# Performance work log

Measured on AMD Instinct MI355X. Metric: run time of the kernel, lower is better.

The kernel has to match this reference:

```python
import jax, jax.numpy as jnp
import numpy as np

B, N_L, C, NH = 8, 256, 256, 8
HH, WW = 64, 64
N_C = HH * WW
L = 3  # focal_level
KS = [3, 5, 7]  # focal kernel sizes: focal_factor*k + focal_window
HD = C // NH
SCALE = HD ** -0.5


def _dwconv(x, w, k):
    # x: [B,C,H,W], w: [C,1,k,k] depthwise (groups=C)
    p = k // 2
    return jax.lax.conv_general_dilated(
        x, w, window_strides=(1, 1), padding=[(p, p), (p, p)],
        feature_group_count=C,
        dimension_numbers=('NCHW', 'OIHW', 'NCHW'))


def setup_inputs() -> dict:
    key = jax.random.key(0)
    ks = jax.random.split(key, 16)
    s = 0.02
    inp = {
        'latents': jax.random.normal(ks[0], (B, N_L, C), jnp.float32),
        'context': jax.random.normal(ks[1], (B, N_C, C), jnp.float32),
        'q_w': jax.random.normal(ks[2], (C, C), jnp.float32) * s,
        'k_w': jax.random.normal(ks[3], (C, C), jnp.float32) * s,
        'f_w': jax.random.normal(ks[4], (C + L + 1, C), jnp.float32) * s,
        'f_b': jnp.zeros((C + L + 1,), jnp.float32),
        'h_w': jax.random.normal(ks[5], (C, C), jnp.float32) * s,
        'h_b': jnp.zeros((C,), jnp.float32),
        'fk0': jax.random.normal(ks[6], (C, 1, KS[0], KS[0]), jnp.float32) * s,
        'fk1': jax.random.normal(ks[7], (C, 1, KS[1], KS[1]), jnp.float32) * s,
        'fk2': jax.random.normal(ks[8], (C, 1, KS[2], KS[2]), jnp.float32) * s,
        'proj_w': jax.random.normal(ks[9], (C, C), jnp.float32) * s,
        'proj_b': jnp.zeros((C,), jnp.float32),
        'H': HH,
        'W': WW,
    }
    return inp


def reference(latents, context, q_w, k_w, f_w, f_b, h_w, h_b,
              fk0, fk1, fk2, proj_w, proj_b, H, W):
    gelu = lambda x: jax.nn.gelu(x, approximate=False)
    # attention scores
    q = (latents @ q_w.T).reshape(B, N_L, NH, HD).transpose(0, 2, 1, 3)  # [B,NH,Nl,HD]
    k = (context @ k_w.T).reshape(B, N_C, NH, HD).transpose(0, 2, 1, 3)  # [B,NH,Nc,HD]
    attn = jax.nn.softmax(jnp.einsum('bhnd,bhmd->bhnm', q, k) * SCALE, axis=-1)
    # focal modulation on context
    f_out = context.reshape(B, H, W, C) @ f_w.T + f_b          # [B,H,W,C+L+1]
    f_out = f_out.transpose(0, 3, 1, 2)                        # [B,C+L+1,H,W]
    v_ctx, gates = f_out[:, :C], f_out[:, C:]
    v_ctx_all = jnp.zeros_like(v_ctx)
    for l, fk in enumerate((fk0, fk1, fk2)):
        v_ctx = gelu(_dwconv(v_ctx, fk, KS[l]))
        v_ctx_all = v_ctx_all + v_ctx * gates[:, l:l + 1]
    v_global = gelu(v_ctx.mean(axis=(2, 3), keepdims=True))
    v_ctx_all = v_ctx_all + v_global * gates[:, L:L + 1]
    # 1x1 conv modulator
    v_mod = jnp.einsum('bchw,dc->bdhw', v_ctx_all, h_w) + h_b[None, :, None, None]
    # NOTE: faithful to original -- raw reshape of NCHW tensor (no permute)
    v = v_mod.reshape(B, N_C, NH, HD).transpose(0, 2, 1, 3)    # [B,NH,Nc,HD]
    out = jnp.einsum('bhnm,bhmd->bhnd', attn, v)               # [B,NH,Nl,HD]
    out = out.transpose(0, 2, 1, 3).reshape(B, N_L, C)
    out = out @ proj_w.T + proj_b
    return out, attn
```

## Files before the change

kernel.cpp:

```cpp
#include <hip/hip_runtime.h>
#include <math.h>


namespace {

constexpr float CSCALE = 0.17677669529663688f;

typedef __attribute__((ext_vector_type(8))) __bf16 bf16x8;
typedef __attribute__((ext_vector_type(4))) float f32x4;

__device__ __forceinline__ float gelu_f(float x) {
  return 0.5f * x * (1.0f + erff(x * 0.70710678118654752f));
}

__device__ __forceinline__ unsigned short f2bf(float f) {
  union { float f; unsigned u; } v; v.f = f;
  unsigned r = v.u + 0x7fffu + ((v.u >> 16) & 1u);
  return (unsigned short)(r >> 16);
}

__device__ __forceinline__ float bf2f(unsigned short u) {
  union { unsigned u; float f; } v; v.u = (unsigned)u << 16;
  return v.f;
}

__device__ __forceinline__ bf16x8 pack8(float4 a, float4 b) {
  union { unsigned short u[8]; bf16x8 v; } A;
  A.u[0] = f2bf(a.x); A.u[1] = f2bf(a.y); A.u[2] = f2bf(a.z); A.u[3] = f2bf(a.w);
  A.u[4] = f2bf(b.x); A.u[5] = f2bf(b.y); A.u[6] = f2bf(b.z); A.u[7] = f2bf(b.w);
  return A.v;
}

__global__ __launch_bounds__(256) void cast_w(
    const float* __restrict__ qw, const float* __restrict__ kw,
    const float* __restrict__ fw, const float* __restrict__ hww,
    const float* __restrict__ pw,
    unsigned short* qwb, unsigned short* kwb, unsigned short* fwb,
    unsigned short* hwb, unsigned short* pwb) {
  const int blk = blockIdx.x;
  const float* s; unsigned short* d; int b0, nq;
  if      (blk < 16) { s = qw;  d = qwb; b0 = blk;      nq = 16384; }
  else if (blk < 32) { s = kw;  d = kwb; b0 = blk - 16; nq = 16384; }
  else if (blk < 49) { s = fw;  d = fwb; b0 = blk - 32; nq = 16640; }
  else if (blk < 65) { s = hww; d = hwb; b0 = blk - 49; nq = 16384; }
  else               { s = pw;  d = pwb; b0 = blk - 65; nq = 16384; }
  #pragma unroll
  for (int t = 0; t < 4; ++t) {
    const int q = b0*1024 + t*256 + threadIdx.x;
    if (q < nq) {
      float4 v = ((const float4*)s)[q];
      ushort4 o;
      o.x = f2bf(v.x); o.y = f2bf(v.y); o.z = f2bf(v.z); o.w = f2bf(v.w);
      ((ushort4*)d)[q] = o;
    }
  }
}

__global__ __launch_bounds__(256) void mfma_proj_rw(
    const float* __restrict__ A, const unsigned short* __restrict__ W,
    unsigned short* __restrict__ out) {
  const int r0 = blockIdx.x * 64;
  const int tid = threadIdx.x, w = tid >> 6, l = tid & 63;
  const int lr = l & 15, lk = l >> 4;
  const int rw = r0 + w*16;
  const float* ap = A + (size_t)(rw + lr)*256 + lk*8;
  f32x4 acc[16];
  #pragma unroll
  for (int j = 0; j < 16; ++j) acc[j] = (f32x4){0.f,0.f,0.f,0.f};
  #pragma unroll
  for (int k0 = 0; k0 < 256; k0 += 32) {
    float4 c0 = *(const float4*)(ap + k0);
    float4 c1 = *(const float4*)(ap + k0 + 4);
    bf16x8 a = pack8(c0, c1);
    #pragma unroll
    for (int j = 0; j < 16; ++j) {
      bf16x8 b = *reinterpret_cast<const bf16x8*>(W + (size_t)(j*16 + lr)*256 + k0 + lk*8);
      acc[j] = __builtin_amdgcn_mfma_f32_16x16x32_bf16(a, b, acc[j], 0, 0, 0);
    }
  }
  #pragma unroll
  for (int j = 0; j < 16; ++j)
    #pragma unroll
    for (int rr = 0; rr < 4; ++rr)
      out[(size_t)(rw + lk*4 + rr)*256 + j*16 + lr] = f2bf(acc[j][rr]);
}

__global__ __launch_bounds__(256) void mfma_f(
    const float* __restrict__ A, const unsigned short* __restrict__ W,
    const float* __restrict__ fb, unsigned short* __restrict__ vctx,
    float* __restrict__ gates) {
  const int r0 = blockIdx.x * 64;
  const int tid = threadIdx.x, w = tid >> 6, l = tid & 63;
  const int lr = l & 15, lk = l >> 4;
  const int rw = r0 + w*16;
  const float* ap = A + (size_t)(rw + lr)*256 + lk*8;
  f32x4 acc[17];
  #pragma unroll
  for (int j = 0; j < 17; ++j) acc[j] = (f32x4){0.f,0.f,0.f,0.f};
  #pragma unroll
  for (int k0 = 0; k0 < 256; k0 += 32) {
    float4 c0 = *(const float4*)(ap + k0);
    float4 c1 = *(const float4*)(ap + k0 + 4);
    bf16x8 a = pack8(c0, c1);
    #pragma unroll
    for (int j = 0; j < 17; ++j) {
      const int n = j*16 + lr;
      bf16x8 b = {};
      if (n < 260)
        b = *reinterpret_cast<const bf16x8*>(W + (size_t)n*256 + k0 + lk*8);
      acc[j] = __builtin_amdgcn_mfma_f32_16x16x32_bf16(a, b, acc[j], 0, 0, 0);
    }
  }
  const int rbase = rw + lk*4;
  const int b = rbase >> 12, hw = rbase & 4095;
  #pragma unroll
  for (int j = 0; j < 17; ++j) {
    const int n = j*16 + lr;
    if (n >= 260) continue;
    const float bb = fb[n];
    if (n < 256) {
      ushort4 o;
      o.x = f2bf(acc[j][0] + bb); o.y = f2bf(acc[j][1] + bb);
      o.z = f2bf(acc[j][2] + bb); o.w = f2bf(acc[j][3] + bb);
      *(ushort4*)&vctx[((size_t)(b*256 + n))*4096 + hw] = o;
    } else {
      float4 o = make_float4(acc[j][0] + bb, acc[j][1] + bb,
                             acc[j][2] + bb, acc[j][3] + bb);
      *(float4*)&gates[((size_t)(b*4 + (n - 256)))*4096 + hw] = o;
    }
  }
}

__global__ __launch_bounds__(256) void fused_conv(
    const unsigned short* in, const float* __restrict__ wk3,
    const float* __restrict__ wk5, const float* __restrict__ wk7,
    const float* __restrict__ gates, unsigned short* out) {
  constexpr int TW = 70;
  __shared__ float A[TW * TW];
  __shared__ float w3[9];
  __shared__ float w5[25];
  __shared__ float w7[49];
  __shared__ float red[4];
  const int tid = threadIdx.x;
  const int b = blockIdx.x >> 8, c = blockIdx.x & 255;
  if (tid < 9)  w3[tid] = wk3[c*9  + tid];
  else if (tid < 34) w5[tid-9]  = wk5[c*25 + tid-9];
  else if (tid < 83) w7[tid-34] = wk7[c*49 + tid-34];
  const unsigned short* ip = in + (size_t)(b*256 + c) * 4096;
  for (int idx = tid; idx < TW*TW; idx += 256) {
    const int ty = idx / TW, tx = idx - ty*TW;
    const int gy = ty - 3, gx = tx - 3;
    A[idx] = (gy >= 0 && gy < 64 && gx >= 0 && gx < 64) ? bf2f(ip[gy*64 + gx]) : 0.0f;
  }
  __syncthreads();
  const float* g0 = gates + (size_t)(b*4 + 0) * 4096;
  const float* g1 = gates + (size_t)(b*4 + 1) * 4096;
  const float* g2 = gates + (size_t)(b*4 + 2) * 4096;
  const float* g3 = gates + (size_t)(b*4 + 3) * 4096;
  float v[16], acc[16];
  #pragma unroll
  for (int ii = 0; ii < 16; ++ii) {
    const int pix = ii*256 + tid;
    const int y = pix >> 6, x = pix & 63;
    float s = 0.f;
    #pragma unroll
    for (int ky = 0; ky < 3; ++ky)
      #pragma unroll
      for (int kx = 0; kx < 3; ++kx)
        s += w3[ky*3 + kx] * A[(y+2+ky)*TW + (x+2+kx)];
    v[ii] = gelu_f(s);
    acc[ii] = v[ii] * g0[pix];
  }
  __syncthreads();
  #pragma unroll
  for (int ii = 0; ii < 16; ++ii) {
    const int pix = ii*256 + tid;
    A[((pix >> 6) + 3)*TW + (pix & 63) + 3] = v[ii];
  }
  __syncthreads();
  #pragma unroll
  for (int ii = 0; ii < 16; ++ii) {
    const int pix = ii*256 + tid;
    const int y = pix >> 6, x = pix & 63;
    float s = 0.f;
    #pragma unroll
    for (int ky = 0; ky < 5; ++ky)
      #pragma unroll
      for (int kx = 0; kx < 5; ++kx)
        s += w5[ky*5 + kx] * A[(y+1+ky)*TW + (x+1+kx)];
    v[ii] = gelu_f(s);
    acc[ii] += v[ii] * g1[pix];
  }
  __syncthreads();
  #pragma unroll
  for (int ii = 0; ii < 16; ++ii) {
    const int pix = ii*256 + tid;
    A[((pix >> 6) + 3)*TW + (pix & 63) + 3] = v[ii];
  }
  __syncthreads();
  float msum = 0.f;
  #pragma unroll
  for (int ii = 0; ii < 16; ++ii) {
    const int pix = ii*256 + tid;
    const int y = pix >> 6, x = pix & 63;
    float s = 0.f;
    #pragma unroll
    for (int ky = 0; ky < 7; ++ky)
      #pragma unroll
      for (int kx = 0; kx < 7; ++kx)
        s += w7[ky*7 + kx] * A[(y+ky)*TW + (x+kx)];
    v[ii] = gelu_f(s);
    acc[ii] += v[ii] * g2[pix];
    msum += v[ii];
  }
  #pragma unroll
  for (int off = 32; off >= 1; off >>= 1) msum += __shfl_xor(msum, off, 64);
  if ((tid & 63) == 0) red[tid >> 6] = msum;
  __syncthreads();
  const float vg = gelu_f((red[0]+red[1]+red[2]+red[3]) * (1.0f/4096.0f));
  unsigned short* vp = out + (size_t)(b*256 + c) * 4096;
  #pragma unroll
  for (int ii = 0; ii < 16; ++ii) {
    const int pix = ii*256 + tid;
    vp[pix] = f2bf(acc[ii] + vg * g3[pix]);
  }
}

__global__ __launch_bounds__(256) void mfma_h(
    const unsigned short* __restrict__ vall, const unsigned short* __restrict__ hwb,
    const float* __restrict__ hb, unsigned short* __restrict__ vlin) {
  __shared__ unsigned short sh[256 * 72];
  const int hw0 = blockIdx.x * 64, b = blockIdx.y;
  const int tid = threadIdx.x, w = tid >> 6, l = tid & 63;
  const int lr = l & 15, lk = l >> 4;
  const int cl = tid >> 3, hl = (tid & 7) * 8;
  #pragma unroll
  for (int c0 = 0; c0 < 256; c0 += 32) {
    const unsigned short* sp = vall + (size_t)(b*256 + c0 + cl)*4096 + hw0 + hl;
    ushort4 u0 = *(const ushort4*)sp;
    ushort4 u1 = *(const ushort4*)(sp + 4);
    sh[(hl+0)*264 + c0+cl] = u0.x; sh[(hl+1)*264 + c0+cl] = u0.y;
    sh[(hl+2)*264 + c0+cl] = u0.z; sh[(hl+3)*264 + c0+cl] = u0.w;
    sh[(hl+4)*264 + c0+cl] = u1.x; sh[(hl+5)*264 + c0+cl] = u1.y;
    sh[(hl+6)*264 + c0+cl] = u1.z; sh[(hl+7)*264 + c0+cl] = u1.w;
  }
  __syncthreads();
  const int dw = w * 64;
  f32x4 acc[4][4];
  #pragma unroll
  for (int j2 = 0; j2 < 4; ++j2)
    #pragma unroll
    for (int j = 0; j < 4; ++j) acc[j2][j] = (f32x4){0.f,0.f,0.f,0.f};
  #pragma unroll
  for (int k0 = 0; k0 < 256; k0 += 32) {
    bf16x8 a[4];
    #pragma unroll
    for (int j2 = 0; j2 < 4; ++j2)
      a[j2] = *reinterpret_cast<const bf16x8*>(hwb + (size_t)(dw + j2*16 + lr)*256 + k0 + lk*8);
    #pragma unroll
    for (int j = 0; j < 4; ++j) {
      bf16x8 bv = *reinterpret_cast<const bf16x8*>(&sh[(j*16 + lr)*264 + k0 + lk*8]);
      #pragma unroll
      for (int j2 = 0; j2 < 4; ++j2)
        acc[j2][j] = __builtin_amdgcn_mfma_f32_16x16x32_bf16(a[j2], bv, acc[j2][j], 0, 0, 0);
    }
  }
  float hbv[4][4];
  #pragma unroll
  for (int j2 = 0; j2 < 4; ++j2)
    #pragma unroll
    for (int rr = 0; rr < 4; ++rr) hbv[j2][rr] = hb[dw + j2*16 + lk*4 + rr];
  __syncthreads();
  #pragma unroll
  for (int j2 = 0; j2 < 4; ++j2)
    #pragma unroll
    for (int j = 0; j < 4; ++j)
      #pragma unroll
      for (int rr = 0; rr < 4; ++rr)
        sh[(dw + j2*16 + lk*4 + rr)*72 + j*16 + lr] = f2bf(acc[j2][j][rr] + hbv[j2][rr]);
  __syncthreads();
  const int q = hw0 >> 8, dim0 = hw0 & 255;
  #pragma unroll
  for (int it = 0; it < 8; ++it) {
    const int dl = it*32 + (tid >> 3);
    const int ch = tid & 7;
    const int m = dl*16 + q;
    uint4 v = *(const uint4*)&sh[dl*72 + ch*8];
    *(uint4*)&vlin[((size_t)(b*4096 + m))*256 + dim0 + ch*8] = v;
  }
}

__global__ __launch_bounds__(256) void trans_bf(
    const unsigned short* __restrict__ vlin, unsigned short* __restrict__ vt) {
  __shared__ unsigned short T[64][72];
  const int tid = threadIdx.x;
  const int m0 = blockIdx.x * 64, d0 = blockIdx.y * 64, b = blockIdx.z;
  #pragma unroll
  for (int it = 0; it < 2; ++it) {
    const int ml = it*32 + (tid >> 3);
    const int ch = tid & 7;
    uint4 v = *(const uint4*)&vlin[((size_t)(b*4096 + m0 + ml))*256 + d0 + ch*8];
    *(uint4*)&T[ml][ch*8] = v;
  }
  __syncthreads();
  #pragma unroll
  for (int it = 0; it < 2; ++it) {
    const int dl = it*32 + (tid >> 3);
    const int ch = tid & 7;
    unsigned short tmp[8];
    #pragma unroll
    for (int k = 0; k < 8; ++k) tmp[k] = T[ch*8 + k][dl];
    *(uint4*)&vt[((size_t)(b*256 + d0 + dl))*4096 + m0 + ch*8] = *(uint4*)tmp;
  }
}

__global__ __launch_bounds__(256) void attn_pv(
    const unsigned short* __restrict__ qb, const unsigned short* __restrict__ kb,
    const unsigned short* __restrict__ vt, float* __restrict__ attn,
    unsigned short* __restrict__ aout) {
  const int blk = blockIdx.x;
  const int bh = blk & 63, nt = blk >> 6;
  const int b = bh >> 3, h = bh & 7;
  const int tid = threadIdx.x;
  const int w = tid >> 6, l = tid & 63;
  const int lr = l & 15, lk = l >> 4;
  const int n0 = nt * 16;
  __shared__ float rs[4][16];
  __shared__ unsigned short pl[4][16][40];
  __shared__ float ps[4][16][36];
  __shared__ float osum[4][16][32];
  bf16x8 aq = *reinterpret_cast<const bf16x8*>(
      qb + ((size_t)(b*256 + n0 + lr))*256 + h*32 + lk*8);
  const unsigned short* kbase = kb + (size_t)b*4096*256 + h*32 + lk*8;
  float sum[4] = {0.f, 0.f, 0.f, 0.f};
  #pragma unroll 2
  for (int mt = 0; mt < 64; ++mt) {
    const int m0 = w*1024 + mt*16;
    bf16x8 bk = *reinterpret_cast<const bf16x8*>(kbase + (size_t)(m0 + lr)*256);
    f32x4 d = __builtin_amdgcn_mfma_f32_16x16x32_bf16(aq, bk, (f32x4){0.f,0.f,0.f,0.f}, 0, 0, 0);
    #pragma unroll
    for (int r = 0; r < 4; ++r) sum[r] += __expf(d[r] * CSCALE);
  }
  #pragma unroll
  for (int r = 0; r < 4; ++r) {
    #pragma unroll
    for (int m = 1; m < 16; m <<= 1) sum[r] += __shfl_xor(sum[r], m, 64);
  }
  if (lr == 0) {
    #pragma unroll
    for (int r = 0; r < 4; ++r) rs[w][lk*4 + r] = sum[r];
  }
  __syncthreads();
  float invS[4];
  #pragma unroll
  for (int r = 0; r < 4; ++r) {
    const int rowi = lk*4 + r;
    invS[r] = 1.0f / (rs[0][rowi] + rs[1][rowi] + rs[2][rowi] + rs[3][rowi]);
  }
  float* ab = attn + ((size_t)bh*256 + n0) * 4096;
  const unsigned short* vb = vt + ((size_t)(b*256 + h*32))*4096;
  const int fr = l >> 3;
  const int fm = (l & 7) * 4;
  f32x4 acc0 = {0.f,0.f,0.f,0.f}, acc1 = {0.f,0.f,0.f,0.f};
  for (int mt = 0; mt < 64; ++mt) {
    const int m0 = w*1024 + mt*16;
    bf16x8 bk = *reinterpret_cast<const bf16x8*>(kbase + (size_t)(m0 + lr)*256);
    f32x4 d = __builtin_amdgcn_mfma_f32_16x16x32_bf16(aq, bk, (f32x4){0.f,0.f,0.f,0.f}, 0, 0, 0);
    const int mo = (mt & 1) << 4;
    #pragma unroll
    for (int r = 0; r < 4; ++r) {
      const float p = __expf(d[r] * CSCALE) * invS[r];
      ps[w][lk*4 + r][mo + lr] = p;
      pl[w][lk*4 + r][mo + lr] = f2bf(p);
    }
    if (mt & 1) {
      const int mb = w*1024 + (mt - 1)*16;
      bf16x8 pa = *reinterpret_cast<const bf16x8*>(&pl[w][lr][lk*8]);
      bf16x8 bv0 = *reinterpret_cast<const bf16x8*>(vb + (size_t)lr*4096 + mb + lk*8);
      bf16x8 bv1 = *reinterpret_cast<const bf16x8*>(vb + (size_t)(16 + lr)*4096 + mb + lk*8);
      acc0 = __builtin_amdgcn_mfma_f32_16x16x32_bf16(pa, bv0, acc0, 0, 0, 0);
      acc1 = __builtin_amdgcn_mfma_f32_16x16x32_bf16(pa, bv1, acc1, 0, 0, 0);
      #pragma unroll
      for (int i = 0; i < 2; ++i) {
        const int row = i*8 + fr;
        float4 pv4 = *(const float4*)&ps[w][row][fm];
        *(float4*)&ab[(size_t)row*4096 + mb + fm] = pv4;
      }
    }
  }
  #pragma unroll
  for (int r = 0; r < 4; ++r) {
    osum[w][lk*4 + r][lr]      = acc0[r];
    osum[w][lk*4 + r][16 + lr] = acc1[r];
  }
  __syncthreads();
  for (int i = tid; i < 512; i += 256) {
    const int n = i >> 5, d = i & 31;
    const float s = osum[0][n][d] + osum[1][n][d] + osum[2][n][d] + osum[3][n][d];
    aout[((size_t)(b*256 + n0 + n))*256 + h*32 + d] = f2bf(s);
  }
}

__global__ __launch_bounds__(256) void mfma_proj(
    const unsigned short* __restrict__ A, const unsigned short* __restrict__ W,
    const float* __restrict__ pb, float* __restrict__ out) {
  const int r0 = blockIdx.x * 64, n0 = blockIdx.y * 64;
  const int tid = threadIdx.x, w = tid >> 6, l = tid & 63;
  const int lr = l & 15, lk = l >> 4;
  const int rw = r0 + w*16;
  const unsigned short* ap = A + (size_t)(rw + lr)*256 + lk*8;
  f32x4 acc[4] = {{0.f,0.f,0.f,0.f},{0.f,0.f,0.f,0.f},{0.f,0.f,0.f,0.f},{0.f,0.f,0.f,0.f}};
  #pragma unroll
  for (int k0 = 0; k0 < 256; k0 += 32) {
    bf16x8 a = *reinterpret_cast<const bf16x8*>(ap + k0);
    #pragma unroll
    for (int j = 0; j < 4; ++j) {
      bf16x8 b = *reinterpret_cast<const bf16x8*>(W + (size_t)(n0 + j*16 + lr)*256 + k0 + lk*8);
      acc[j] = __builtin_amdgcn_mfma_f32_16x16x32_bf16(a, b, acc[j], 0, 0, 0);
    }
  }
  #pragma unroll
  for (int j = 0; j < 4; ++j) {
    const int n = n0 + j*16 + lr;
    const float bb = pb[n];
    #pragma unroll
    for (int rr = 0; rr < 4; ++rr)
      out[(size_t)(rw + lk*4 + rr)*256 + n] = acc[j][rr] + bb;
  }
}

}

extern "C" void kernel_launch(void* const* d_in, const int* in_sizes, int n_in,
                              void* d_out, int out_size, void* d_ws, size_t ws_size,
                              hipStream_t stream) {
  (void)in_sizes; (void)n_in; (void)out_size; (void)ws_size;
  const float* latents = (const float*)d_in[0];
  const float* context = (const float*)d_in[1];
  const float* q_w    = (const float*)d_in[2];
  const float* k_w    = (const float*)d_in[3];
  const float* f_w    = (const float*)d_in[4];
  const float* f_b    = (const float*)d_in[5];
  const float* h_w    = (const float*)d_in[6];
  const float* h_b    = (const float*)d_in[7];
  const float* fk0    = (const float*)d_in[8];
  const float* fk1    = (const float*)d_in[9];
  const float* fk2    = (const float*)d_in[10];
  const float* proj_w = (const float*)d_in[11];
  const float* proj_b = (const float*)d_in[12];

  float* out0 = (float*)d_out;
  float* attn = out0 + (size_t)8*256*256;

  char* w = (char*)d_ws;
  unsigned short* vcv     = (unsigned short*)(w + 0x0);
  unsigned short* k_bf    = (unsigned short*)(w + 0x1000000);
  unsigned short* v_tb    = (unsigned short*)(w + 0x2000000);
  unsigned short* vlin_bf = (unsigned short*)(w + 0x3000000);
  unsigned short* q_bf    = (unsigned short*)(w + 0x4000000);
  unsigned short* aout_bf = (unsigned short*)(w + 0x4100000);
  unsigned short* qw_bf   = (unsigned short*)(w + 0x4200000);
  unsigned short* kw_bf   = (unsigned short*)(w + 0x4220000);
  unsigned short* fw_bf   = (unsigned short*)(w + 0x4240000);
  unsigned short* hw_bf   = (unsigned short*)(w + 0x4270000);
  unsigned short* pw_bf   = (unsigned short*)(w + 0x4290000);
  float*          gates   = (float*)(w + 0x42B0000);

  cast_w<<<81, 256, 0, stream>>>(q_w, k_w, f_w, h_w, proj_w,
                                 qw_bf, kw_bf, fw_bf, hw_bf, pw_bf);
  mfma_proj_rw<<<32,  256, 0, stream>>>(latents, qw_bf, q_bf);
  mfma_proj_rw<<<512, 256, 0, stream>>>(context, kw_bf, k_bf);
  mfma_f   <<<512, 256, 0, stream>>>(context, fw_bf, f_b, vcv, gates);
  fused_conv<<<2048, 256, 0, stream>>>(vcv, fk0, fk1, fk2, gates, vcv);
  mfma_h   <<<dim3(64, 8), 256, 0, stream>>>(vcv, hw_bf, h_b, vlin_bf);
  trans_bf <<<dim3(64, 4, 8), 256, 0, stream>>>(vlin_bf, v_tb);
  attn_pv  <<<1024, 256, 0, stream>>>(q_bf, k_bf, v_tb, attn, aout_bf);
  mfma_proj<<<dim3(32, 4), 256, 0, stream>>>(aout_bf, pw_bf, proj_b, out0);
}
```

Measured before the change: 350.1 us.

## Store K head-planar, stage mfma_f output through LDS, register-block conv columns

The K projection now writes a per-head planar layout [b,h,m,32], so attention reads each K row with a 64-byte stride instead of a 512-byte stride. mfma_f stages the bf16 v_ctx tile in shared memory so it can write coalesced 16-byte rows instead of scattered ushort4 stores. The depthwise conv kernel gives each thread a 16-row vertical strip and slides down each kernel column, so every loaded shared-memory value feeds several outputs and fewer LDS reads are needed. These add shared-memory use and more live registers in the conv.

Result: slower. 358.3 us (+2.3%).

```diff
diff --git a/kernel.cpp b/kernel.cpp
--- a/kernel.cpp
+++ b/kernel.cpp
@@ -85,10 +85,50 @@
       out[(size_t)(rw + lk*4 + rr)*256 + j*16 + lr] = f2bf(acc[j][rr]);
 }
 
+__global__ __launch_bounds__(256) void mfma_kproj(
+    const float* __restrict__ A, const unsigned short* __restrict__ W,
+    unsigned short* __restrict__ kpl) {
+  __shared__ unsigned short sh[64 * 264];
+  const int r0 = blockIdx.x * 64;
+  const int tid = threadIdx.x, w = tid >> 6, l = tid & 63;
+  const int lr = l & 15, lk = l >> 4;
+  const int rw = r0 + w*16;
+  const float* ap = A + (size_t)(rw + lr)*256 + lk*8;
+  f32x4 acc[16];
+  #pragma unroll
+  for (int j = 0; j < 16; ++j) acc[j] = (f32x4){0.f,0.f,0.f,0.f};
+  #pragma unroll
+  for (int k0 = 0; k0 < 256; k0 += 32) {
+    float4 c0 = *(const float4*)(ap + k0);
+    float4 c1 = *(const float4*)(ap + k0 + 4);
+    bf16x8 a = pack8(c0, c1);
+    #pragma unroll
+    for (int j = 0; j < 16; ++j) {
+      bf16x8 b = *reinterpret_cast<const bf16x8*>(W + (size_t)(j*16 + lr)*256 + k0 + lk*8);
+      acc[j] = __builtin_amdgcn_mfma_f32_16x16x32_bf16(a, b, acc[j], 0, 0, 0);
+    }
+  }
+  #pragma unroll
+  for (int j = 0; j < 16; ++j)
+    #pragma unroll
+    for (int rr = 0; rr < 4; ++rr)
+      sh[(w*16 + lk*4 + rr)*264 + j*16 + lr] = f2bf(acc[j][rr]);
+  __syncthreads();
+  const int b = r0 >> 12, mm0 = r0 & 4095;
+  #pragma unroll
+  for (int it = 0; it < 8; ++it) {
+    const int idx = it*256 + tid;
+    const int ch = idx & 3, m = (idx >> 2) & 63, h = idx >> 8;
+    uint4 v = *(const uint4*)&sh[m*264 + h*32 + ch*8];
+    *(uint4*)&kpl[(((size_t)(b*8 + h))*4096 + mm0 + m)*32 + ch*8] = v;
+  }
+}
+
 __global__ __launch_bounds__(256) void mfma_f(
     const float* __restrict__ A, const unsigned short* __restrict__ W,
     const float* __restrict__ fb, unsigned short* __restrict__ vctx,
     float* __restrict__ gates) {
+  __shared__ unsigned short sh[256 * 68];
   const int r0 = blockIdx.x * 64;
   const int tid = threadIdx.x, w = tid >> 6, l = tid & 63;
   const int lr = l & 15, lk = l >> 4;
@@ -111,23 +151,32 @@
       acc[j] = __builtin_amdgcn_mfma_f32_16x16x32_bf16(a, b, acc[j], 0, 0, 0);
     }
   }
-  const int rbase = rw + lk*4;
-  const int b = rbase >> 12, hw = rbase & 4095;
-  #pragma unroll
-  for (int j = 0; j < 17; ++j) {
-    const int n = j*16 + lr;
-    if (n >= 260) continue;
-    const float bb = fb[n];
-    if (n < 256) {
-      ushort4 o;
-      o.x = f2bf(acc[j][0] + bb); o.y = f2bf(acc[j][1] + bb);
-      o.z = f2bf(acc[j][2] + bb); o.w = f2bf(acc[j][3] + bb);
-      *(ushort4*)&vctx[((size_t)(b*256 + n))*4096 + hw] = o;
-    } else {
-      float4 o = make_float4(acc[j][0] + bb, acc[j][1] + bb,
-                             acc[j][2] + bb, acc[j][3] + bb);
-      *(float4*)&gates[((size_t)(b*4 + (n - 256)))*4096 + hw] = o;
-    }
+  const int hwl = w*16 + lk*4;
+  #pragma unroll
+  for (int j = 0; j < 16; ++j) {
+    const float bb = fb[j*16 + lr];
+    #pragma unroll
+    for (int rr = 0; rr < 4; ++rr)
+      sh[(j*16 + lr)*68 + hwl + rr] = f2bf(acc[j][rr] + bb);
+  }
+  {
+    const int rbase = rw + lk*4;
+    const int b = rbase >> 12, hw = rbase & 4095;
+    if (lr < 4) {
+      const float bb = fb[256 + lr];
+      float4 o = make_float4(acc[16][0] + bb, acc[16][1] + bb,
+                             acc[16][2] + bb, acc[16][3] + bb);
+      *(float4*)&gates[((size_t)(b*4 + lr))*4096 + hw] = o;
+    }
+  }
+  __syncthreads();
+  const int b = r0 >> 12, hw0 = r0 & 4095;
+  #pragma unroll
+  for (int it = 0; it < 8; ++it) {
+    const int idx = it*256 + tid;
+    const int n = idx >> 3, ch = idx & 7;
+    uint4 v = *(const uint4*)&sh[n*68 + ch*8];
+    *(uint4*)&vctx[((size_t)(b*256 + n))*4096 + hw0 + ch*8] = v;
   }
 }
 
@@ -153,65 +202,81 @@
     A[idx] = (gy >= 0 && gy < 64 && gx >= 0 && gx < 64) ? bf2f(ip[gy*64 + gx]) : 0.0f;
   }
   __syncthreads();
+  const int x = tid & 63, ys = (tid >> 6) * 16;
   const float* g0 = gates + (size_t)(b*4 + 0) * 4096;
   const float* g1 = gates + (size_t)(b*4 + 1) * 4096;
   const float* g2 = gates + (size_t)(b*4 + 2) * 4096;
   const float* g3 = gates + (size_t)(b*4 + 3) * 4096;
-  float v[16], acc[16];
-  #pragma unroll
-  for (int ii = 0; ii < 16; ++ii) {
-    const int pix = ii*256 + tid;
-    const int y = pix >> 6, x = pix & 63;
-    float s = 0.f;
-    #pragma unroll
-    for (int ky = 0; ky < 3; ++ky)
+  float s[16], acc[16];
+  #pragma unroll
+  for (int i = 0; i < 16; ++i) s[i] = 0.f;
+  #pragma unroll
+  for (int kx = 0; kx < 3; ++kx) {
+    const float* col = &A[(ys + 2)*TW + x + 2 + kx];
+    #pragma unroll
+    for (int r = 0; r < 18; ++r) {
+      const float v = col[r*TW];
       #pragma unroll
-      for (int kx = 0; kx < 3; ++kx)
-        s += w3[ky*3 + kx] * A[(y+2+ky)*TW + (x+2+kx)];
-    v[ii] = gelu_f(s);
-    acc[ii] = v[ii] * g0[pix];
-  }
-  __syncthreads();
-  #pragma unroll
-  for (int ii = 0; ii < 16; ++ii) {
-    const int pix = ii*256 + tid;
-    A[((pix >> 6) + 3)*TW + (pix & 63) + 3] = v[ii];
-  }
-  __syncthreads();
-  #pragma unroll
-  for (int ii = 0; ii < 16; ++ii) {
-    const int pix = ii*256 + tid;
-    const int y = pix >> 6, x = pix & 63;
-    float s = 0.f;
-    #pragma unroll
-    for (int ky = 0; ky < 5; ++ky)
+      for (int ky = 0; ky < 3; ++ky) {
+        const int i = r - ky;
+        if (i >= 0 && i < 16) s[i] += w3[ky*3 + kx] * v;
+      }
+    }
+  }
+  #pragma unroll
+  for (int i = 0; i < 16; ++i) {
+    s[i] = gelu_f(s[i]);
+    acc[i] = s[i] * g0[(ys + i)*64 + x];
+  }
+  __syncthreads();
+  #pragma unroll
+  for (int i = 0; i < 16; ++i) A[(ys + i + 3)*TW + x + 3] = s[i];
+  __syncthreads();
+  #pragma unroll
+  for (int i = 0; i < 16; ++i) s[i] = 0.f;
+  #pragma unroll
+  for (int kx = 0; kx < 5; ++kx) {
+    const float* col = &A[(ys + 1)*TW + x + 1 + kx];
+    #pragma unroll
+    for (int r = 0; r < 20; ++r) {
+      const float v = col[r*TW];
       #pragma unroll
-      for (int kx = 0; kx < 5; ++kx)
-        s += w5[ky*5 + kx] * A[(y+1+ky)*TW + (x+1+kx)];
-    v[ii] = gelu_f(s);
-    acc[ii] += v[ii] * g1[pix];
-  }
-  __syncthreads();
-  #pragma unroll
-  for (int ii = 0; ii < 16; ++ii) {
-    const int pix = ii*256 + tid;
-    A[((pix >> 6) + 3)*TW + (pix & 63) + 3] = v[ii];
-  }
-  __syncthreads();
+      for (int ky = 0; ky < 5; ++ky) {
+        const int i = r - ky;
+        if (i >= 0 && i < 16) s[i] += w5[ky*5 + kx] * v;
+      }
+    }
+  }
+  #pragma unroll
+  for (int i = 0; i < 16; ++i) {
+    s[i] = gelu_f(s[i]);
+    acc[i] += s[i] * g1[(ys + i)*64 + x];
+  }
+  __syncthreads();
+  #pragma unroll
+  for (int i = 0; i < 16; ++i) A[(ys + i + 3)*TW + x + 3] = s[i];
+  __syncthreads();
+  #pragma unroll
+  for (int i = 0; i < 16; ++i) s[i] = 0.f;
+  #pragma unroll
+  for (int kx = 0; kx < 7; ++kx) {
+    const float* col = &A[ys*TW + x + kx];
+    #pragma unroll
+    for (int r = 0; r < 22; ++r) {
+      const float v = col[r*TW];
+      #pragma unroll
+      for (int ky = 0; ky < 7; ++ky) {
+        const int i = r - ky;
+        if (i >= 0 && i < 16) s[i] += w7[ky*7 + kx] * v;
+      }
+    }
+  }
   float msum = 0.f;
   #pragma unroll
-  for (int ii = 0; ii < 16; ++ii) {
-    const int pix = ii*256 + tid;
-    const int y = pix >> 6, x = pix & 63;
-    float s = 0.f;
-    #pragma unroll
-    for (int ky = 0; ky < 7; ++ky)
-      #pragma unroll
-      for (int kx = 0; kx < 7; ++kx)
-        s += w7[ky*7 + kx] * A[(y+ky)*TW + (x+kx)];
-    v[ii] = gelu_f(s);
-    acc[ii] += v[ii] * g2[pix];
-    msum += v[ii];
+  for (int i = 0; i < 16; ++i) {
+    s[i] = gelu_f(s[i]);
+    acc[i] += s[i] * g2[(ys + i)*64 + x];
+    msum += s[i];
   }
   #pragma unroll
   for (int off = 32; off >= 1; off >>= 1) msum += __shfl_xor(msum, off, 64);
@@ -220,9 +285,9 @@
   const float vg = gelu_f((red[0]+red[1]+red[2]+red[3]) * (1.0f/4096.0f));
   unsigned short* vp = out + (size_t)(b*256 + c) * 4096;
   #pragma unroll
-  for (int ii = 0; ii < 16; ++ii) {
-    const int pix = ii*256 + tid;
-    vp[pix] = f2bf(acc[ii] + vg * g3[pix]);
+  for (int i = 0; i < 16; ++i) {
+    const int pix = (ys + i)*64 + x;
+    vp[pix] = f2bf(acc[i] + vg * g3[pix]);
   }
 }
 
@@ -315,7 +380,7 @@
 }
 
 __global__ __launch_bounds__(256) void attn_pv(
-    const unsigned short* __restrict__ qb, const unsigned short* __restrict__ kb,
+    const unsigned short* __restrict__ qb, const unsigned short* __restrict__ kpl,
     const unsigned short* __restrict__ vt, float* __restrict__ attn,
     unsigned short* __restrict__ aout) {
   const int blk = blockIdx.x;
@@ -331,12 +396,12 @@
   __shared__ float osum[4][16][32];
   bf16x8 aq = *reinterpret_cast<const bf16x8*>(
       qb + ((size_t)(b*256 + n0 + lr))*256 + h*32 + lk*8);
-  const unsigned short* kbase = kb + (size_t)b*4096*256 + h*32 + lk*8;
+  const unsigned short* kbase = kpl + ((size_t)(b*8 + h))*4096*32 + lk*8;
   float sum[4] = {0.f, 0.f, 0.f, 0.f};
   #pragma unroll 2
   for (int mt = 0; mt < 64; ++mt) {
     const int m0 = w*1024 + mt*16;
-    bf16x8 bk = *reinterpret_cast<const bf16x8*>(kbase + (size_t)(m0 + lr)*256);
+    bf16x8 bk = *reinterpret_cast<const bf16x8*>(kbase + (size_t)(m0 + lr)*32);
     f32x4 d = __builtin_amdgcn_mfma_f32_16x16x32_bf16(aq, bk, (f32x4){0.f,0.f,0.f,0.f}, 0, 0, 0);
     #pragma unroll
     for (int r = 0; r < 4; ++r) sum[r] += __expf(d[r] * CSCALE);
@@ -364,7 +429,7 @@
   f32x4 acc0 = {0.f,0.f,0.f,0.f}, acc1 = {0.f,0.f,0.f,0.f};
   for (int mt = 0; mt < 64; ++mt) {
     const int m0 = w*1024 + mt*16;
-    bf16x8 bk = *reinterpret_cast<const bf16x8*>(kbase + (size_t)(m0 + lr)*256);
+    bf16x8 bk = *reinterpret_cast<const bf16x8*>(kbase + (size_t)(m0 + lr)*32);
     f32x4 d = __builtin_amdgcn_mfma_f32_16x16x32_bf16(aq, bk, (f32x4){0.f,0.f,0.f,0.f}, 0, 0, 0);
     const int mo = (mt & 1) << 4;
     #pragma unroll
@@ -454,7 +519,7 @@
 
   char* w = (char*)d_ws;
   unsigned short* vcv     = (unsigned short*)(w + 0x0);
-  unsigned short* k_bf    = (unsigned short*)(w + 0x1000000);
+  unsigned short* kpl     = (unsigned short*)(w + 0x1000000);
   unsigned short* v_tb    = (unsigned short*)(w + 0x2000000);
   unsigned short* vlin_bf = (unsigned short*)(w + 0x3000000);
   unsigned short* q_bf    = (unsigned short*)(w + 0x4000000);
@@ -469,11 +534,11 @@
   cast_w<<<81, 256, 0, stream>>>(q_w, k_w, f_w, h_w, proj_w,
                                  qw_bf, kw_bf, fw_bf, hw_bf, pw_bf);
   mfma_proj_rw<<<32,  256, 0, stream>>>(latents, qw_bf, q_bf);
-  mfma_proj_rw<<<512, 256, 0, stream>>>(context, kw_bf, k_bf);
-  mfma_f   <<<512, 256, 0, stream>>>(context, fw_bf, f_b, vcv, gates);
-  fused_conv<<<2048, 256, 0, stream>>>(vcv, fk0, fk1, fk2, gates, vcv);
-  mfma_h   <<<dim3(64, 8), 256, 0, stream>>>(vcv, hw_bf, h_b, vlin_bf);
-  trans_bf <<<dim3(64, 4, 8), 256, 0, stream>>>(vlin_bf, v_tb);
-  attn_pv  <<<1024, 256, 0, stream>>>(q_bf, k_bf, v_tb, attn, aout_bf);
-  mfma_proj<<<dim3(32, 4), 256, 0, stream>>>(aout_bf, pw_bf, proj_b, out0);
-}
+  mfma_kproj  <<<512, 256, 0, stream>>>(context, kw_bf, kpl);
+  mfma_f      <<<512, 256, 0, stream>>>(context, fw_bf, f_b, vcv, gates);
+  fused_conv  <<<2048, 256, 0, stream>>>(vcv, fk0, fk1, fk2, gates, vcv);
+  mfma_h      <<<dim3(64, 8), 256, 0, stream>>>(vcv, hw_bf, h_b, vlin_bf);
+  trans_bf    <<<dim3(64, 4, 8), 256, 0, stream>>>(vlin_bf, v_tb);
+  attn_pv     <<<1024, 256, 0, stream>>>(q_bf, kpl, v_tb, attn, aout_bf);
+  mfma_proj   <<<dim3(32, 4), 256, 0, stream>>>(aout_bf, pw_bf, proj_b, out0);
+}
```
